# Kernel optimization log

Measured on AMD Instinct MI355X. Metric: run time of the kernel, lower is better.

The kernel has to match this reference:

```python
import jax, jax.numpy as jnp
import numpy as np

BETA = 0.25

def setup_inputs() -> dict:
    key = jax.random.key(0)
    k1, k2 = jax.random.split(key)
    z = jax.random.normal(k1, (32, 64, 64, 64), dtype=jnp.float32)  # (B, D, H, W)
    # EmbeddingEMA init: uniform(-1/K, 1/K)
    K, D = 1024, 64
    weight = jax.random.uniform(k2, (K, D), dtype=jnp.float32, minval=-1.0 / K, maxval=1.0 / K)
    return {"z": z, "weight": weight}


def reference(z, weight):
    b, d, h, w = z.shape
    K = weight.shape[0]
    # permute (B,D,H,W) -> (B,H,W,D) and flatten to (N, D)
    z_flat = jnp.transpose(z, (0, 2, 3, 1)).reshape(-1, d)
    # squared euclidean distance: ||z||^2 + ||c||^2 - 2 z c^T  -> (N, K)
    distance = (
        jnp.sum(z_flat * z_flat, axis=1, keepdims=True)
        + jnp.sum(weight * weight, axis=1)
        - 2.0 * jnp.matmul(z_flat, weight.T)
    )
    vq_indices = jnp.argmin(distance, axis=1)  # (N,)
    z_quantized = weight[vq_indices]  # gather (N, D)
    # one-hot scatter stats (training-time EMA inputs)
    vq_current_count = jax.ops.segment_sum(
        jnp.ones((z_flat.shape[0],), dtype=z_flat.dtype), vq_indices, num_segments=K)
    vq_current_sum = jax.ops.segment_sum(z_flat, vq_indices, num_segments=K)  # (K, D)
    commitment_loss = jnp.mean((z_flat - jax.lax.stop_gradient(z_quantized)) ** 2)
    loss = BETA * commitment_loss
    # straight-through estimator
    q = z_flat + jax.lax.stop_gradient(z_quantized - z_flat)
    q = jnp.transpose(q.reshape(b, h, w, d), (0, 3, 1, 2))  # back to (B, D, H, W)
    return q, loss, commitment_loss, vq_current_count, vq_current_sum
```

## Files before the change

kernel.cpp:

```cpp
#include <hip/hip_runtime.h>


#define HWsz   4096
#define Dd     64
#define Kk     1024
#define NB     32
#define NTOT   131072
#define QSIZE  (NTOT * Dd)
#define BETA_C 0.25f

typedef float  f32x4  __attribute__((ext_vector_type(4)));
typedef short  bf16x8 __attribute__((ext_vector_type(8)));

__device__ __forceinline__ unsigned short f2bf(float f) {
    unsigned u = __float_as_uint(f);
    u += 0x7FFF + ((u >> 16) & 1);
    return (unsigned short)(u >> 16);
}
__device__ __forceinline__ float bf2f(unsigned short b) {
    return __uint_as_float(((unsigned)b) << 16);
}

__global__ __launch_bounds__(256) void c2_kernel(const float* __restrict__ w,
                                                 float* __restrict__ c2) {
    int k = blockIdx.x * 256 + threadIdx.x;
    const float4* c4 = reinterpret_cast<const float4*>(w + k * Dd);
    float s0 = 0.f, s1 = 0.f, s2 = 0.f, s3 = 0.f;
#pragma unroll
    for (int q = 0; q < 16; ++q) {
        float4 cq = c4[q];
        s0 = fmaf(cq.x, cq.x, s0); s1 = fmaf(cq.y, cq.y, s1);
        s2 = fmaf(cq.z, cq.z, s2); s3 = fmaf(cq.w, cq.w, s3);
    }
    c2[k] = (s0 + s1) + (s2 + s3);
}

__global__ __launch_bounds__(256) void wsplit_kernel(const float* __restrict__ w,
                                                     unsigned short* __restrict__ whi,
                                                     unsigned short* __restrict__ wlo) {
    int t = blockIdx.x * 256 + threadIdx.x;
    int k = t >> 6, d = t & 63;
    float v = w[t];
    unsigned short hb = f2bf(v);
    unsigned short lb = f2bf(v - bf2f(hb));
    int ctile = k >> 4, col = k & 15;
    int s = d >> 5, kg = (d >> 3) & 3, j = d & 7;
    int idx = (((ctile * 2 + s) * 64) + kg * 16 + col) * 8 + j;
    whi[idx] = hb; wlo[idx] = lb;
}

__global__ __launch_bounds__(256) void vq_dist(const float* __restrict__ z,
                                               const float* __restrict__ w,
                                               const float* __restrict__ c2,
                                               const unsigned short* __restrict__ whi,
                                               const unsigned short* __restrict__ wlo,
                                               float* __restrict__ out,
                                               float* __restrict__ accum,
                                               int* __restrict__ idx_ws) {
    const int lane = threadIdx.x & 63;
    const int wid  = threadIdx.x >> 6;
    const int rt   = blockIdx.x * 4 + wid;
    const int b    = rt >> 8;
    const int hw0  = (rt & 255) << 4;
    const int col  = lane & 15;
    const int kg   = lane >> 4;

    const float* zbase = z + (size_t)b * (Dd * HWsz) + hw0 + col;
    float zv[16];
#pragma unroll
    for (int s = 0; s < 2; ++s)
#pragma unroll
        for (int j = 0; j < 8; ++j)
            zv[s * 8 + j] = zbase[(size_t)(32 * s + kg * 8 + j) * HWsz];

    bf16x8 zhi[2], zlo[2];
#pragma unroll
    for (int s = 0; s < 2; ++s) {
        bf16x8 h, l;
#pragma unroll
        for (int j = 0; j < 8; ++j) {
            unsigned short hb = f2bf(zv[s * 8 + j]);
            unsigned short lb = f2bf(zv[s * 8 + j] - bf2f(hb));
            h[j] = (short)hb; l[j] = (short)lb;
        }
        zhi[s] = h; zlo[s] = l;
    }

    float best0 = 3.4e38f, best1 = 3.4e38f, best2 = 3.4e38f, best3 = 3.4e38f;
    int   bk0 = 0, bk1 = 0, bk2 = 0, bk3 = 0;

    const bf16x8* ph = reinterpret_cast<const bf16x8*>(whi);
    const bf16x8* pl = reinterpret_cast<const bf16x8*>(wlo);

#pragma unroll 2
    for (int ct = 0; ct < 64; ++ct) {
        bf16x8 wh0 = ph[(ct * 2 + 0) * 64 + lane];
        bf16x8 wh1 = ph[(ct * 2 + 1) * 64 + lane];
        bf16x8 wl0 = pl[(ct * 2 + 0) * 64 + lane];
        bf16x8 wl1 = pl[(ct * 2 + 1) * 64 + lane];

        f32x4 za = {0.f, 0.f, 0.f, 0.f};
        f32x4 zb = {0.f, 0.f, 0.f, 0.f};
        za = __builtin_amdgcn_mfma_f32_16x16x32_bf16(zhi[0], wh0, za, 0, 0, 0);
        za = __builtin_amdgcn_mfma_f32_16x16x32_bf16(zhi[1], wh1, za, 0, 0, 0);
        za = __builtin_amdgcn_mfma_f32_16x16x32_bf16(zhi[0], wl0, za, 0, 0, 0);
        za = __builtin_amdgcn_mfma_f32_16x16x32_bf16(zhi[1], wl1, za, 0, 0, 0);
        zb = __builtin_amdgcn_mfma_f32_16x16x32_bf16(zlo[0], wh0, zb, 0, 0, 0);
        zb = __builtin_amdgcn_mfma_f32_16x16x32_bf16(zlo[1], wh1, zb, 0, 0, 0);

        float cv = c2[ct * 16 + col];
        int   kc = ct * 16 + col;
        { float s = fmaf(-2.f, za[0] + zb[0], cv); if (s < best0) { best0 = s; bk0 = kc; } }
        { float s = fmaf(-2.f, za[1] + zb[1], cv); if (s < best1) { best1 = s; bk1 = kc; } }
        { float s = fmaf(-2.f, za[2] + zb[2], cv); if (s < best2) { best2 = s; bk2 = kc; } }
        { float s = fmaf(-2.f, za[3] + zb[3], cv); if (s < best3) { best3 = s; bk3 = kc; } }
    }

    float best[4] = {best0, best1, best2, best3};
    int   bk[4]   = {bk0, bk1, bk2, bk3};
#pragma unroll
    for (int off = 1; off < 16; off <<= 1) {
#pragma unroll
        for (int r = 0; r < 4; ++r) {
            float ob = __shfl_xor(best[r], off, 64);
            int   ok = __shfl_xor(bk[r],   off, 64);
            if (ob < best[r] || (ob == best[r] && ok < bk[r])) { best[r] = ob; bk[r] = ok; }
        }
    }

    int srcl = (col >> 2) << 4;
    int c0 = __shfl(bk[0], srcl, 64);
    int c1 = __shfl(bk[1], srcl, 64);
    int c2r = __shfl(bk[2], srcl, 64);
    int c3 = __shfl(bk[3], srcl, 64);
    int rsel = col & 3;
    int mybk = (rsel == 0) ? c0 : (rsel == 1) ? c1 : (rsel == 2) ? c2r : c3;

    if (lane < 16) idx_ws[(size_t)b * HWsz + hw0 + col] = mybk;

    float cb[16];
#pragma unroll
    for (int s = 0; s < 2; ++s) {
        const float4* cw = reinterpret_cast<const float4*>(w + mybk * Dd + 32 * s + kg * 8);
        float4 p0 = cw[0], p1 = cw[1];
        cb[s * 8 + 0] = p0.x; cb[s * 8 + 1] = p0.y; cb[s * 8 + 2] = p0.z; cb[s * 8 + 3] = p0.w;
        cb[s * 8 + 4] = p1.x; cb[s * 8 + 5] = p1.y; cb[s * 8 + 6] = p1.z; cb[s * 8 + 7] = p1.w;
    }

    float* qbase = out + (size_t)b * (Dd * HWsz) + hw0 + col;
    float commit = 0.f;
#pragma unroll
    for (int s = 0; s < 2; ++s)
#pragma unroll
        for (int j = 0; j < 8; ++j) {
            int   d  = 32 * s + kg * 8 + j;
            float zz = zv[s * 8 + j];
            float cc = cb[s * 8 + j];
            qbase[(size_t)d * HWsz] = zz + (cc - zz);
            float dd = zz - cc;
            commit = fmaf(dd, dd, commit);
        }

#pragma unroll
    for (int off = 32; off > 0; off >>= 1) commit += __shfl_down(commit, off, 64);

    __shared__ float red[4];
    if (lane == 0) red[wid] = commit;
    __syncthreads();
    if (threadIdx.x == 0)
        atomicAdd(accum, (red[0] + red[1]) + (red[2] + red[3]));
}

__global__ __launch_bounds__(256) void vq_stats(const float* __restrict__ z,
                                                const int* __restrict__ idx_ws,
                                                float* __restrict__ psum,
                                                float* __restrict__ pcnt) {
    const int bd = blockIdx.x;
    const int b = bd >> 6, d = bd & 63;
    const bool docnt = (d == 0);

    __shared__ float acc[Kk];
    __shared__ float cnt[Kk];
    for (int i = threadIdx.x; i < Kk; i += 256) { acc[i] = 0.f; cnt[i] = 0.f; }
    __syncthreads();

    const int4*   ip = reinterpret_cast<const int4*>(idx_ws + (size_t)b * HWsz);
    const float4* zp = reinterpret_cast<const float4*>(z + ((size_t)b * Dd + d) * HWsz);
#pragma unroll
    for (int c = threadIdx.x; c < HWsz / 4; c += 256) {
        int4   k4 = ip[c];
        float4 v4 = zp[c];
        atomicAdd(&acc[k4.x], v4.x);
        atomicAdd(&acc[k4.y], v4.y);
        atomicAdd(&acc[k4.z], v4.z);
        atomicAdd(&acc[k4.w], v4.w);
        if (docnt) {
            atomicAdd(&cnt[k4.x], 1.f);
            atomicAdd(&cnt[k4.y], 1.f);
            atomicAdd(&cnt[k4.z], 1.f);
            atomicAdd(&cnt[k4.w], 1.f);
        }
    }
    __syncthreads();

    float* po = psum + (size_t)bd * Kk;
    for (int i = threadIdx.x; i < Kk; i += 256) po[i] = acc[i];
    if (docnt) {
        float* pc = pcnt + (size_t)b * Kk;
        for (int i = threadIdx.x; i < Kk; i += 256) pc[i] = cnt[i];
    }
}

__global__ __launch_bounds__(256) void vq_reduce(const float* __restrict__ psum,
                                                 const float* __restrict__ pcnt,
                                                 float* __restrict__ out) {
    int t = blockIdx.x * 256 + threadIdx.x;
    int k = t & 1023, d = t >> 10;
    float s = 0.f;
#pragma unroll
    for (int b = 0; b < NB; ++b)
        s += psum[(((size_t)b * Dd + d) << 10) + k];
    out[QSIZE + 2 + Kk + (size_t)k * Dd + d] = s;
    if (t < Kk) {
        float c = 0.f;
#pragma unroll
        for (int b = 0; b < NB; ++b) c += pcnt[((size_t)b << 10) + t];
        out[QSIZE + 2 + t] = c;
    }
}

__global__ void vq_finish(const float* __restrict__ accum, float* __restrict__ out) {
    float c = accum[0] / (float)QSIZE;
    out[QSIZE]     = BETA_C * c;
    out[QSIZE + 1] = c;
}

extern "C" void kernel_launch(void* const* d_in, const int* in_sizes, int n_in,
                              void* d_out, int out_size, void* d_ws, size_t ws_size,
                              hipStream_t stream) {
    const float* z = (const float*)d_in[0];
    const float* w = (const float*)d_in[1];
    float* out = (float*)d_out;

    float* accum = (float*)d_ws;
    float* c2    = (float*)d_ws + 64;
    unsigned short* whi = (unsigned short*)((float*)d_ws + 64 + Kk);
    unsigned short* wlo = whi + (Kk * Dd);
    int*   idx_ws = (int*)(wlo + (Kk * Dd));
    float* psum   = (float*)(idx_ws + NTOT);
    float* pcnt   = psum + (size_t)NB * Dd * Kk;

    hipMemsetAsync(accum, 0, 64 * sizeof(float), stream);

    c2_kernel<<<Kk / 256, 256, 0, stream>>>(w, c2);
    wsplit_kernel<<<(Kk * Dd) / 256, 256, 0, stream>>>(w, whi, wlo);
    vq_dist<<<NTOT / 64, 256, 0, stream>>>(z, w, c2, whi, wlo, out, accum, idx_ws);
    vq_stats<<<NB * Dd, 256, 0, stream>>>(z, idx_ws, psum, pcnt);
    vq_reduce<<<(Kk * Dd) / 256, 256, 0, stream>>>(psum, pcnt, out);
    vq_finish<<<1, 1, 0, stream>>>(accum, out);
}
```

Before: 262.5 us.

## Register-block four row tiles per wave in VQ distance kernel and fuse small kernels

Each wave now processes four 16-row tiles of z against every codebook tile, so each loaded bf16 codebook fragment is reused across four MFMA groups instead of one. This cuts repeated codebook loads in the main distance loop. The stats kernel now handles eight D channels per block, reusing the loaded index vector, and the c2/wsplit and reduce/finish kernels are merged to remove launches. The costs are higher register pressure, fewer blocks (512 distance blocks, 256 stats blocks) that may lower occupancy, and a 32KB shared accumulator in the stats kernel. The z value is also rebuilt from hi+lo bf16 parts, which may not exactly match the original fp32 values.

```diff
diff --git a/kernel.cpp b/kernel.cpp
--- a/kernel.cpp
+++ b/kernel.cpp
@@ -21,23 +21,10 @@
     return __uint_as_float(((unsigned)b) << 16);
 }
 
-__global__ __launch_bounds__(256) void c2_kernel(const float* __restrict__ w,
-                                                 float* __restrict__ c2) {
-    int k = blockIdx.x * 256 + threadIdx.x;
-    const float4* c4 = reinterpret_cast<const float4*>(w + k * Dd);
-    float s0 = 0.f, s1 = 0.f, s2 = 0.f, s3 = 0.f;
-#pragma unroll
-    for (int q = 0; q < 16; ++q) {
-        float4 cq = c4[q];
-        s0 = fmaf(cq.x, cq.x, s0); s1 = fmaf(cq.y, cq.y, s1);
-        s2 = fmaf(cq.z, cq.z, s2); s3 = fmaf(cq.w, cq.w, s3);
-    }
-    c2[k] = (s0 + s1) + (s2 + s3);
-}
-
-__global__ __launch_bounds__(256) void wsplit_kernel(const float* __restrict__ w,
-                                                     unsigned short* __restrict__ whi,
-                                                     unsigned short* __restrict__ wlo) {
+__global__ __launch_bounds__(256) void vq_prep(const float* __restrict__ w,
+                                               float* __restrict__ c2,
+                                               unsigned short* __restrict__ whi,
+                                               unsigned short* __restrict__ wlo) {
     int t = blockIdx.x * 256 + threadIdx.x;
     int k = t >> 6, d = t & 63;
     float v = w[t];
@@ -47,6 +34,18 @@
     int s = d >> 5, kg = (d >> 3) & 3, j = d & 7;
     int idx = (((ctile * 2 + s) * 64) + kg * 16 + col) * 8 + j;
     whi[idx] = hb; wlo[idx] = lb;
+
+    if (t < Kk) {
+        const float4* c4 = reinterpret_cast<const float4*>(w + t * Dd);
+        float s0 = 0.f, s1 = 0.f, s2 = 0.f, s3 = 0.f;
+#pragma unroll
+        for (int q = 0; q < 16; ++q) {
+            float4 cq = c4[q];
+            s0 = fmaf(cq.x, cq.x, s0); s1 = fmaf(cq.y, cq.y, s1);
+            s2 = fmaf(cq.z, cq.z, s2); s3 = fmaf(cq.w, cq.w, s3);
+        }
+        c2[t] = (s0 + s1) + (s2 + s3);
+    }
 }
 
 __global__ __launch_bounds__(256) void vq_dist(const float* __restrict__ z,
@@ -59,107 +58,113 @@
                                                int* __restrict__ idx_ws) {
     const int lane = threadIdx.x & 63;
     const int wid  = threadIdx.x >> 6;
-    const int rt   = blockIdx.x * 4 + wid;
-    const int b    = rt >> 8;
-    const int hw0  = (rt & 255) << 4;
+    const int b    = blockIdx.x >> 4;
+    const int t0   = (blockIdx.x & 15) * 16 + wid * 4;
     const int col  = lane & 15;
     const int kg   = lane >> 4;
 
-    const float* zbase = z + (size_t)b * (Dd * HWsz) + hw0 + col;
-    float zv[16];
-#pragma unroll
-    for (int s = 0; s < 2; ++s)
-#pragma unroll
-        for (int j = 0; j < 8; ++j)
-            zv[s * 8 + j] = zbase[(size_t)(32 * s + kg * 8 + j) * HWsz];
-
-    bf16x8 zhi[2], zlo[2];
-#pragma unroll
-    for (int s = 0; s < 2; ++s) {
-        bf16x8 h, l;
-#pragma unroll
-        for (int j = 0; j < 8; ++j) {
-            unsigned short hb = f2bf(zv[s * 8 + j]);
-            unsigned short lb = f2bf(zv[s * 8 + j] - bf2f(hb));
-            h[j] = (short)hb; l[j] = (short)lb;
-        }
-        zhi[s] = h; zlo[s] = l;
-    }
-
-    float best0 = 3.4e38f, best1 = 3.4e38f, best2 = 3.4e38f, best3 = 3.4e38f;
-    int   bk0 = 0, bk1 = 0, bk2 = 0, bk3 = 0;
+    bf16x8 zhi[4][2], zlo[4][2];
+#pragma unroll
+    for (int m = 0; m < 4; ++m) {
+        const int hw0 = (t0 + m) << 4;
+        const float* zbase = z + (size_t)b * (Dd * HWsz) + hw0 + col;
+#pragma unroll
+        for (int s = 0; s < 2; ++s) {
+            bf16x8 h, l;
+#pragma unroll
+            for (int j = 0; j < 8; ++j) {
+                float zz = zbase[(size_t)(32 * s + kg * 8 + j) * HWsz];
+                unsigned short hb = f2bf(zz);
+                unsigned short lb = f2bf(zz - bf2f(hb));
+                h[j] = (short)hb; l[j] = (short)lb;
+            }
+            zhi[m][s] = h; zlo[m][s] = l;
+        }
+    }
+
+    float best[4][4];
+    int   bk[4][4];
+#pragma unroll
+    for (int m = 0; m < 4; ++m)
+#pragma unroll
+        for (int r = 0; r < 4; ++r) { best[m][r] = 3.4e38f; bk[m][r] = 0; }
 
     const bf16x8* ph = reinterpret_cast<const bf16x8*>(whi);
     const bf16x8* pl = reinterpret_cast<const bf16x8*>(wlo);
 
-#pragma unroll 2
     for (int ct = 0; ct < 64; ++ct) {
         bf16x8 wh0 = ph[(ct * 2 + 0) * 64 + lane];
         bf16x8 wh1 = ph[(ct * 2 + 1) * 64 + lane];
         bf16x8 wl0 = pl[(ct * 2 + 0) * 64 + lane];
         bf16x8 wl1 = pl[(ct * 2 + 1) * 64 + lane];
 
-        f32x4 za = {0.f, 0.f, 0.f, 0.f};
-        f32x4 zb = {0.f, 0.f, 0.f, 0.f};
-        za = __builtin_amdgcn_mfma_f32_16x16x32_bf16(zhi[0], wh0, za, 0, 0, 0);
-        za = __builtin_amdgcn_mfma_f32_16x16x32_bf16(zhi[1], wh1, za, 0, 0, 0);
-        za = __builtin_amdgcn_mfma_f32_16x16x32_bf16(zhi[0], wl0, za, 0, 0, 0);
-        za = __builtin_amdgcn_mfma_f32_16x16x32_bf16(zhi[1], wl1, za, 0, 0, 0);
-        zb = __builtin_amdgcn_mfma_f32_16x16x32_bf16(zlo[0], wh0, zb, 0, 0, 0);
-        zb = __builtin_amdgcn_mfma_f32_16x16x32_bf16(zlo[1], wh1, zb, 0, 0, 0);
-
         float cv = c2[ct * 16 + col];
         int   kc = ct * 16 + col;
-        { float s = fmaf(-2.f, za[0] + zb[0], cv); if (s < best0) { best0 = s; bk0 = kc; } }
-        { float s = fmaf(-2.f, za[1] + zb[1], cv); if (s < best1) { best1 = s; bk1 = kc; } }
-        { float s = fmaf(-2.f, za[2] + zb[2], cv); if (s < best2) { best2 = s; bk2 = kc; } }
-        { float s = fmaf(-2.f, za[3] + zb[3], cv); if (s < best3) { best3 = s; bk3 = kc; } }
-    }
-
-    float best[4] = {best0, best1, best2, best3};
-    int   bk[4]   = {bk0, bk1, bk2, bk3};
+
+#pragma unroll
+        for (int m = 0; m < 4; ++m) {
+            f32x4 za = {0.f, 0.f, 0.f, 0.f};
+            f32x4 zb = {0.f, 0.f, 0.f, 0.f};
+            za = __builtin_amdgcn_mfma_f32_16x16x32_bf16(zhi[m][0], wh0, za, 0, 0, 0);
+            za = __builtin_amdgcn_mfma_f32_16x16x32_bf16(zhi[m][1], wh1, za, 0, 0, 0);
+            za = __builtin_amdgcn_mfma_f32_16x16x32_bf16(zhi[m][0], wl0, za, 0, 0, 0);
+            za = __builtin_amdgcn_mfma_f32_16x16x32_bf16(zhi[m][1], wl1, za, 0, 0, 0);
+            zb = __builtin_amdgcn_mfma_f32_16x16x32_bf16(zlo[m][0], wh0, zb, 0, 0, 0);
+            zb = __builtin_amdgcn_mfma_f32_16x16x32_bf16(zlo[m][1], wh1, zb, 0, 0, 0);
+#pragma unroll
+            for (int r = 0; r < 4; ++r) {
+                float s = fmaf(-2.f, za[r] + zb[r], cv);
+                if (s < best[m][r]) { best[m][r] = s; bk[m][r] = kc; }
+            }
+        }
+    }
+
 #pragma unroll
     for (int off = 1; off < 16; off <<= 1) {
 #pragma unroll
-        for (int r = 0; r < 4; ++r) {
-            float ob = __shfl_xor(best[r], off, 64);
-            int   ok = __shfl_xor(bk[r],   off, 64);
-            if (ob < best[r] || (ob == best[r] && ok < bk[r])) { best[r] = ob; bk[r] = ok; }
-        }
-    }
-
-    int srcl = (col >> 2) << 4;
-    int c0 = __shfl(bk[0], srcl, 64);
-    int c1 = __shfl(bk[1], srcl, 64);
-    int c2r = __shfl(bk[2], srcl, 64);
-    int c3 = __shfl(bk[3], srcl, 64);
-    int rsel = col & 3;
-    int mybk = (rsel == 0) ? c0 : (rsel == 1) ? c1 : (rsel == 2) ? c2r : c3;
-
-    if (lane < 16) idx_ws[(size_t)b * HWsz + hw0 + col] = mybk;
-
-    float cb[16];
-#pragma unroll
-    for (int s = 0; s < 2; ++s) {
-        const float4* cw = reinterpret_cast<const float4*>(w + mybk * Dd + 32 * s + kg * 8);
-        float4 p0 = cw[0], p1 = cw[1];
-        cb[s * 8 + 0] = p0.x; cb[s * 8 + 1] = p0.y; cb[s * 8 + 2] = p0.z; cb[s * 8 + 3] = p0.w;
-        cb[s * 8 + 4] = p1.x; cb[s * 8 + 5] = p1.y; cb[s * 8 + 6] = p1.z; cb[s * 8 + 7] = p1.w;
-    }
-
-    float* qbase = out + (size_t)b * (Dd * HWsz) + hw0 + col;
+        for (int m = 0; m < 4; ++m)
+#pragma unroll
+            for (int r = 0; r < 4; ++r) {
+                float ob = __shfl_xor(best[m][r], off, 64);
+                int   ok = __shfl_xor(bk[m][r],   off, 64);
+                if (ob < best[m][r] || (ob == best[m][r] && ok < bk[m][r])) {
+                    best[m][r] = ob; bk[m][r] = ok;
+                }
+            }
+    }
+
     float commit = 0.f;
-#pragma unroll
-    for (int s = 0; s < 2; ++s)
-#pragma unroll
-        for (int j = 0; j < 8; ++j) {
-            int   d  = 32 * s + kg * 8 + j;
-            float zz = zv[s * 8 + j];
-            float cc = cb[s * 8 + j];
-            qbase[(size_t)d * HWsz] = zz + (cc - zz);
-            float dd = zz - cc;
-            commit = fmaf(dd, dd, commit);
-        }
+    const int srcl = (col >> 2) << 4;
+    const int rsel = col & 3;
+#pragma unroll
+    for (int m = 0; m < 4; ++m) {
+        int c0 = __shfl(bk[m][0], srcl, 64);
+        int c1 = __shfl(bk[m][1], srcl, 64);
+        int c2r = __shfl(bk[m][2], srcl, 64);
+        int c3 = __shfl(bk[m][3], srcl, 64);
+        int mybk = (rsel == 0) ? c0 : (rsel == 1) ? c1 : (rsel == 2) ? c2r : c3;
+
+        const int hw0 = (t0 + m) << 4;
+        if (lane < 16) idx_ws[(size_t)b * HWsz + hw0 + col] = mybk;
+
+        float* qbase = out + (size_t)b * (Dd * HWsz) + hw0 + col;
+#pragma unroll
+        for (int s = 0; s < 2; ++s) {
+            const float4* cw = reinterpret_cast<const float4*>(w + mybk * Dd + 32 * s + kg * 8);
+            float4 p0 = cw[0], p1 = cw[1];
+            float cb[8] = {p0.x, p0.y, p0.z, p0.w, p1.x, p1.y, p1.z, p1.w};
+#pragma unroll
+            for (int j = 0; j < 8; ++j) {
+                int   d  = 32 * s + kg * 8 + j;
+                float zz = bf2f((unsigned short)zhi[m][s][j]) +
+                           bf2f((unsigned short)zlo[m][s][j]);
+                float cc = cb[j];
+                qbase[(size_t)d * HWsz] = zz + (cc - zz);
+                float dd = zz - cc;
+                commit = fmaf(dd, dd, commit);
+            }
+        }
+    }
 
 #pragma unroll
     for (int off = 32; off > 0; off >>= 1) commit += __shfl_down(commit, off, 64);
@@ -175,25 +180,32 @@
                                                 const int* __restrict__ idx_ws,
                                                 float* __restrict__ psum,
                                                 float* __restrict__ pcnt) {
-    const int bd = blockIdx.x;
-    const int b = bd >> 6, d = bd & 63;
-    const bool docnt = (d == 0);
-
-    __shared__ float acc[Kk];
+    const int b     = blockIdx.x >> 3;
+    const int chunk = blockIdx.x & 7;
+    const int dbase = chunk * 8;
+    const bool docnt = (chunk == 0);
+
+    __shared__ float acc[8][Kk];
     __shared__ float cnt[Kk];
-    for (int i = threadIdx.x; i < Kk; i += 256) { acc[i] = 0.f; cnt[i] = 0.f; }
+    for (int i = threadIdx.x; i < 8 * Kk; i += 256)
+        acc[i >> 10][i & 1023] = 0.f;
+    for (int i = threadIdx.x; i < Kk; i += 256) cnt[i] = 0.f;
     __syncthreads();
 
-    const int4*   ip = reinterpret_cast<const int4*>(idx_ws + (size_t)b * HWsz);
-    const float4* zp = reinterpret_cast<const float4*>(z + ((size_t)b * Dd + d) * HWsz);
-#pragma unroll
-    for (int c = threadIdx.x; c < HWsz / 4; c += 256) {
-        int4   k4 = ip[c];
-        float4 v4 = zp[c];
-        atomicAdd(&acc[k4.x], v4.x);
-        atomicAdd(&acc[k4.y], v4.y);
-        atomicAdd(&acc[k4.z], v4.z);
-        atomicAdd(&acc[k4.w], v4.w);
+    const int4* ip = reinterpret_cast<const int4*>(idx_ws + (size_t)b * HWsz);
+#pragma unroll
+    for (int it = 0; it < 4; ++it) {
+        int c4 = it * 256 + threadIdx.x;
+        int4 k4 = ip[c4];
+#pragma unroll
+        for (int d8 = 0; d8 < 8; ++d8) {
+            const float4 v4 = reinterpret_cast<const float4*>(
+                z + ((size_t)b * Dd + dbase + d8) * HWsz)[c4];
+            atomicAdd(&acc[d8][k4.x], v4.x);
+            atomicAdd(&acc[d8][k4.y], v4.y);
+            atomicAdd(&acc[d8][k4.z], v4.z);
+            atomicAdd(&acc[d8][k4.w], v4.w);
+        }
         if (docnt) {
             atomicAdd(&cnt[k4.x], 1.f);
             atomicAdd(&cnt[k4.y], 1.f);
@@ -203,8 +215,9 @@
     }
     __syncthreads();
 
-    float* po = psum + (size_t)bd * Kk;
-    for (int i = threadIdx.x; i < Kk; i += 256) po[i] = acc[i];
+    float* po = psum + (size_t)b * (Dd * Kk) + (size_t)dbase * Kk;
+    for (int i = threadIdx.x; i < 8 * Kk; i += 256)
+        po[i] = acc[i >> 10][i & 1023];
     if (docnt) {
         float* pc = pcnt + (size_t)b * Kk;
         for (int i = threadIdx.x; i < Kk; i += 256) pc[i] = cnt[i];
@@ -213,13 +226,14 @@
 
 __global__ __launch_bounds__(256) void vq_reduce(const float* __restrict__ psum,
                                                  const float* __restrict__ pcnt,
+                                                 const float* __restrict__ accum,
                                                  float* __restrict__ out) {
     int t = blockIdx.x * 256 + threadIdx.x;
     int k = t & 1023, d = t >> 10;
     float s = 0.f;
 #pragma unroll
     for (int b = 0; b < NB; ++b)
-        s += psum[(((size_t)b * Dd + d) << 10) + k];
+        s += psum[(size_t)b * (Dd * Kk) + (size_t)d * Kk + k];
     out[QSIZE + 2 + Kk + (size_t)k * Dd + d] = s;
     if (t < Kk) {
         float c = 0.f;
@@ -227,12 +241,11 @@
         for (int b = 0; b < NB; ++b) c += pcnt[((size_t)b << 10) + t];
         out[QSIZE + 2 + t] = c;
     }
-}
-
-__global__ void vq_finish(const float* __restrict__ accum, float* __restrict__ out) {
-    float c = accum[0] / (float)QSIZE;
-    out[QSIZE]     = BETA_C * c;
-    out[QSIZE + 1] = c;
+    if (t == 0) {
+        float c = accum[0] / (float)QSIZE;
+        out[QSIZE]     = BETA_C * c;
+        out[QSIZE + 1] = c;
+    }
 }
 
 extern "C" void kernel_launch(void* const* d_in, const int* in_sizes, int n_in,
@@ -252,10 +265,8 @@
 
     hipMemsetAsync(accum, 0, 64 * sizeof(float), stream);
 
-    c2_kernel<<<Kk / 256, 256, 0, stream>>>(w, c2);
-    wsplit_kernel<<<(Kk * Dd) / 256, 256, 0, stream>>>(w, whi, wlo);
-    vq_dist<<<NTOT / 64, 256, 0, stream>>>(z, w, c2, whi, wlo, out, accum, idx_ws);
-    vq_stats<<<NB * Dd, 256, 0, stream>>>(z, idx_ws, psum, pcnt);
-    vq_reduce<<<(Kk * Dd) / 256, 256, 0, stream>>>(psum, pcnt, out);
-    vq_finish<<<1, 1, 0, stream>>>(accum, out);
-}
+    vq_prep<<<(Kk * Dd) / 256, 256, 0, stream>>>(w, c2, whi, wlo);
+    vq_dist<<<NTOT / 256, 256, 0, stream>>>(z, w, c2, whi, wlo, out, accum, idx_ws);
+    vq_stats<<<NB * 8, 256, 0, stream>>>(z, idx_ws, psum, pcnt);
+    vq_reduce<<<(Kk * Dd) / 256, 256, 0, stream>>>(psum, pcnt, accum, out);
+}
```

After: 243.0 us. 7.4% less time.
